# Optimization experiments

Hardware: AMD Instinct MI355X
Metric: run time of the kernel (lower is better)

Reference implementation:

```python
import jax, jax.numpy as jnp
import numpy as np

BN_EPS = 1e-5


def setup_inputs() -> dict:
    key = jax.random.key(0)
    k1, k2, k3 = jax.random.split(key, 3)
    N, C_in, T, V = 32, 64, 288, 25
    C_out = 64
    fv = jax.random.normal(k1, (N, C_in, T, V), dtype=jnp.float32)
    adj = jax.random.uniform(k2, (V, V), dtype=jnp.float32)
    # Conv2d(2*C_in, C_out, 1x1) weight flattened to [C_out, 2*C_in]; kaiming-ish scale
    W = jax.random.normal(k3, (C_out, 2 * C_in), dtype=jnp.float32) * (2.0 / (2 * C_in)) ** 0.5
    b = jnp.zeros((C_out,), dtype=jnp.float32)
    gamma = jnp.ones((C_out,), dtype=jnp.float32)   # bn_init scale=1
    beta = jnp.zeros((C_out,), dtype=jnp.float32)
    return {"fv": fv, "adj": adj, "W": W, "b": b, "gamma": gamma, "beta": beta}


def reference(fv, adj, W, b, gamma, beta):
    # fv: [N, C, T, V]; neighbor aggregation over joints via learnable adjacency
    fv_agg = jnp.einsum('nctv,vy->ncty', fv, adj)
    cat = jnp.concatenate([fv, fv_agg], axis=1)            # [N, 2C, T, V]
    # 1x1 conv == channel matmul
    out = jnp.einsum('ncty,oc->noty', cat, W) + b[None, :, None, None]
    # BatchNorm2d in training mode: batch stats over (N, T, V) per channel
    mean = out.mean(axis=(0, 2, 3), keepdims=True)
    var = out.var(axis=(0, 2, 3), keepdims=True)
    out = (out - mean) * jax.lax.rsqrt(var + BN_EPS)
    out = out * gamma[None, :, None, None] + beta[None, :, None, None]
    return jax.nn.relu(out)
```

## Files before the change

kernel.cpp:

```cpp
#include <hip/hip_runtime.h>

#define N_DIM 32
#define C_IN 64
#define C_OUT 64
#define T_DIM 288
#define V_DIM 25
#define TV 7200
#define NROWS 9216
#define NTV 230400
#define TOTAL 14745600
#define BN_EPS 1e-5f
#define NTILES 1800

#define WS_WINT 0
#define WS_SUM 8192
#define WS_SQ  8256

__global__ __launch_bounds__(256) void prep_kernel(const float* __restrict__ W,
                                                   float* __restrict__ ws) {
  const int i = blockIdx.x * 256 + threadIdx.x;
  if (blockIdx.x == 0 && threadIdx.x < 128) ws[WS_SUM + threadIdx.x] = 0.0f;
  const int s = i & 1;
  const int oo = (i >> 1) & 31;
  const int c = (i >> 6) & 63;
  const int h = i >> 12;
  const int o = h * 32 + oo;
  ws[WS_WINT + i] = W[o * 128 + s * 64 + c];
}

__device__ __forceinline__ float reduce32_lane(float* v, int lane) {
#pragma unroll
  for (int s = 0; s < 5; ++s) {
    const int m = 1 << s;
    const bool up = (lane & m) != 0;
    const int pairs = 32 >> (s + 1);
#pragma unroll
    for (int q = 0; q < pairs; ++q) {
      const float keep = up ? v[2 * q + 1] : v[2 * q];
      const float send = up ? v[2 * q] : v[2 * q + 1];
      const float recv = __shfl_xor(send, m, 64);
      v[q] = keep + recv;
    }
  }
  return v[0];
}

__global__ __launch_bounds__(256, 4) void main_kernel(
    const float* __restrict__ fv, const float* __restrict__ adj,
    const float* __restrict__ wint, float* __restrict__ stats,
    float* __restrict__ out) {
  __shared__ __align__(16) float buf[2][7][36];
  __shared__ float lsum[C_OUT];
  __shared__ float lsq[C_OUT];

  const int tid = threadIdx.x;
  if (tid < 64) { lsum[tid] = 0.0f; lsq[tid] = 0.0f; }

  const int half = __builtin_amdgcn_readfirstlane(tid) >> 7;
  const int lane = tid & 63;
  const float* __restrict__ wbase = wint + half * 4096;

  const int j0 = blockIdx.x << 7;
  const int col = j0 + (tid & 127);
  const int row = col / V_DIM;
  const int y = col - row * V_DIM;
  const int rbase = j0 / V_DIM;
  const int rowoff = row - rbase;

  float adjcol[V_DIM];
#pragma unroll
  for (int v = 0; v < V_DIM; ++v) adjcol[v] = adj[v * V_DIM + y];

  bool stager = false;
  int base_e = 0, srr = 0, sv = 0;
  if (tid < 175) {
    srr = tid / V_DIM;
    sv = tid - srr * V_DIM;
    const int Rg = rbase + srr;
    if (Rg < NROWS) {
      stager = true;
      const int n = Rg / T_DIM;
      const int t = Rg - n * T_DIM;
      base_e = n * (C_IN * TV) + t * V_DIM + sv;
    }
  }

  float acc[32];
#pragma unroll
  for (int oo = 0; oo < 32; ++oo) acc[oo] = 0.0f;

  float r0 = stager ? fv[base_e] : 0.0f;
  float r1 = stager ? fv[base_e + TV] : 0.0f;

#pragma unroll 1
  for (int c = 0; c < C_IN; ++c) {
    if (tid < 175) buf[c & 1][srr][sv] = r0;
    r0 = r1;
    if (stager && c + 2 < C_IN) r1 = fv[base_e + (c + 2) * TV];
    __syncthreads();

    const float* __restrict__ br = &buf[c & 1][rowoff][0];
    const float x = br[y];
    const float4* __restrict__ b4 = reinterpret_cast<const float4*>(br);
    float xa0 = 0.f, xa1 = 0.f, xa2 = 0.f, xa3 = 0.f;
#pragma unroll
    for (int q = 0; q < 6; ++q) {
      const float4 f = b4[q];
      xa0 = fmaf(f.x, adjcol[4 * q + 0], xa0);
      xa1 = fmaf(f.y, adjcol[4 * q + 1], xa1);
      xa2 = fmaf(f.z, adjcol[4 * q + 2], xa2);
      xa3 = fmaf(f.w, adjcol[4 * q + 3], xa3);
    }
    xa0 = fmaf(br[24], adjcol[24], xa0);
    const float xa = (xa0 + xa1) + (xa2 + xa3);

    const float* __restrict__ w = wbase + c * 64;
#pragma unroll
    for (int oo = 0; oo < 32; ++oo)
      acc[oo] = fmaf(x, w[oo * 2], fmaf(xa, w[oo * 2 + 1], acc[oo]));
  }

  {
    const int n = row / T_DIM;
    const int t = row - n * T_DIM;
    float* op = out + ((size_t)n * C_OUT + half * 32) * TV + t * V_DIM + y;
#pragma unroll
    for (int oo = 0; oo < 32; ++oo) op[oo * TV] = acc[oo];
  }

  float sq[32];
#pragma unroll
  for (int i = 0; i < 32; ++i) sq[i] = acc[i] * acc[i];
  float s = reduce32_lane(acc, lane);
  s += __shfl_xor(s, 32, 64);
  float q = reduce32_lane(sq, lane);
  q += __shfl_xor(q, 32, 64);

  if (lane < 32) {
    atomicAdd(&lsum[half * 32 + lane], s);
    atomicAdd(&lsq[half * 32 + lane], q);
  }
  __syncthreads();
  if (tid < 64) {
    atomicAdd(&stats[tid], lsum[tid]);
    atomicAdd(&stats[64 + tid], lsq[tid]);
  }
}

__global__ __launch_bounds__(256) void bn_kernel(const float* __restrict__ stats,
                                                 const float* __restrict__ gamma,
                                                 const float* __restrict__ beta,
                                                 float* __restrict__ out) {
  __shared__ float s_scale[C_OUT];
  __shared__ float s_shift[C_OUT];
  const int tid = threadIdx.x;
  if (tid < C_OUT) {
    const float inv = 1.0f / (float)NTV;
    const float mean = stats[tid] * inv;
    const float var = fmaf(stats[64 + tid], inv, -mean * mean);
    const float sc = gamma[tid] * rsqrtf(var + BN_EPS);
    s_scale[tid] = sc;
    s_shift[tid] = fmaf(-mean, sc, beta[tid]);
  }
  __syncthreads();

  float4* o4 = reinterpret_cast<float4*>(out);
  const int total4 = TOTAL / 4;
  const int stride = gridDim.x * blockDim.x;
  for (int i = blockIdx.x * blockDim.x + tid; i < total4; i += stride) {
    float4 v = o4[i];
    const int o = (i / 1800) & 63;
    const float sc = s_scale[o];
    const float sh = s_shift[o];
    v.x = fmaxf(fmaf(v.x, sc, sh), 0.0f);
    v.y = fmaxf(fmaf(v.y, sc, sh), 0.0f);
    v.z = fmaxf(fmaf(v.z, sc, sh), 0.0f);
    v.w = fmaxf(fmaf(v.w, sc, sh), 0.0f);
    o4[i] = v;
  }
}

extern "C" void kernel_launch(void* const* d_in, const int* in_sizes, int n_in,
                              void* d_out, int out_size, void* d_ws, size_t ws_size,
                              hipStream_t stream) {
  const float* fv = (const float*)d_in[0];
  const float* adj = (const float*)d_in[1];
  const float* W = (const float*)d_in[2];
  const float* gamma = (const float*)d_in[4];
  const float* beta = (const float*)d_in[5];
  float* out = (float*)d_out;
  float* ws = (float*)d_ws;

  hipLaunchKernelGGL(prep_kernel, dim3(32), dim3(256), 0, stream, W, ws);
  hipLaunchKernelGGL(main_kernel, dim3(NTILES), dim3(256), 0, stream,
                     fv, adj, ws + WS_WINT, ws + WS_SUM, out);
  hipLaunchKernelGGL(bn_kernel, dim3(2048), dim3(256), 0, stream,
                     ws + WS_SUM, gamma, beta, out);
}
```

Measured before the change: 298.3 us.

## Stage full per-tile fv slab in LDS once and simplify BN pass indexing

The main kernel no longer double-buffers one channel at a time with a barrier per channel. It now loads all 64 channels of the tile's fv slab into shared memory up front, with a single sync before the compute loop. This removes 64 barriers and exposes more memory-level parallelism, but uses about 50KB of LDS per block and lowers the launch-bounds occupancy hint from 4 to 3. The BN kernel now assigns one (n,channel) plane per block and computes scale and shift per block, dropping the shared-memory table and the per-element divide.

Measured after the change: 286.4 us. -4.0%, faster.

```diff
diff --git a/kernel.cpp b/kernel.cpp
--- a/kernel.cpp
+++ b/kernel.cpp
@@ -11,6 +11,9 @@
 #define TOTAL 14745600
 #define BN_EPS 1e-5f
 #define NTILES 1800
+
+#define ROW_W 28
+#define SLAB_W 196
 
 #define WS_WINT 0
 #define WS_SUM 8192
@@ -45,11 +48,11 @@
   return v[0];
 }
 
-__global__ __launch_bounds__(256, 4) void main_kernel(
+__global__ __launch_bounds__(256, 3) void fused_kernel(
     const float* __restrict__ fv, const float* __restrict__ adj,
     const float* __restrict__ wint, float* __restrict__ stats,
     float* __restrict__ out) {
-  __shared__ __align__(16) float buf[2][7][36];
+  __shared__ __align__(16) float lfv[C_IN * SLAB_W];
   __shared__ float lsum[C_OUT];
   __shared__ float lsq[C_OUT];
 
@@ -61,45 +64,40 @@
   const float* __restrict__ wbase = wint + half * 4096;
 
   const int j0 = blockIdx.x << 7;
+  const int rbase = j0 / V_DIM;
   const int col = j0 + (tid & 127);
   const int row = col / V_DIM;
   const int y = col - row * V_DIM;
-  const int rbase = j0 / V_DIM;
   const int rowoff = row - rbase;
 
   float adjcol[V_DIM];
 #pragma unroll
   for (int v = 0; v < V_DIM; ++v) adjcol[v] = adj[v * V_DIM + y];
 
-  bool stager = false;
-  int base_e = 0, srr = 0, sv = 0;
-  if (tid < 175) {
-    srr = tid / V_DIM;
-    sv = tid - srr * V_DIM;
-    const int Rg = rbase + srr;
+#pragma unroll 1
+  for (int i = tid; i < C_IN * 175; i += 256) {
+    const int c = i / 175;
+    const int rem = i - c * 175;
+    const int rr = rem / V_DIM;
+    const int v = rem - rr * V_DIM;
+    const int Rg = rbase + rr;
+    float val = 0.0f;
     if (Rg < NROWS) {
-      stager = true;
       const int n = Rg / T_DIM;
       const int t = Rg - n * T_DIM;
-      base_e = n * (C_IN * TV) + t * V_DIM + sv;
+      val = fv[n * (C_IN * TV) + c * TV + t * V_DIM + v];
     }
+    lfv[c * SLAB_W + rr * ROW_W + v] = val;
   }
+  __syncthreads();
 
   float acc[32];
 #pragma unroll
   for (int oo = 0; oo < 32; ++oo) acc[oo] = 0.0f;
 
-  float r0 = stager ? fv[base_e] : 0.0f;
-  float r1 = stager ? fv[base_e + TV] : 0.0f;
-
 #pragma unroll 1
   for (int c = 0; c < C_IN; ++c) {
-    if (tid < 175) buf[c & 1][srr][sv] = r0;
-    r0 = r1;
-    if (stager && c + 2 < C_IN) r1 = fv[base_e + (c + 2) * TV];
-    __syncthreads();
-
-    const float* __restrict__ br = &buf[c & 1][rowoff][0];
+    const float* __restrict__ br = &lfv[c * SLAB_W + rowoff * ROW_W];
     const float x = br[y];
     const float4* __restrict__ b4 = reinterpret_cast<const float4*>(br);
     float xa0 = 0.f, xa1 = 0.f, xa2 = 0.f, xa3 = 0.f;
@@ -151,32 +149,22 @@
                                                  const float* __restrict__ gamma,
                                                  const float* __restrict__ beta,
                                                  float* __restrict__ out) {
-  __shared__ float s_scale[C_OUT];
-  __shared__ float s_shift[C_OUT];
-  const int tid = threadIdx.x;
-  if (tid < C_OUT) {
-    const float inv = 1.0f / (float)NTV;
-    const float mean = stats[tid] * inv;
-    const float var = fmaf(stats[64 + tid], inv, -mean * mean);
-    const float sc = gamma[tid] * rsqrtf(var + BN_EPS);
-    s_scale[tid] = sc;
-    s_shift[tid] = fmaf(-mean, sc, beta[tid]);
-  }
-  __syncthreads();
+  const int o = blockIdx.x & 63;
+  const float inv = 1.0f / (float)NTV;
+  const float mean = stats[o] * inv;
+  const float var = fmaf(stats[64 + o], inv, -mean * mean);
+  const float sc = gamma[o] * rsqrtf(var + BN_EPS);
+  const float sh = fmaf(-mean, sc, beta[o]);
 
-  float4* o4 = reinterpret_cast<float4*>(out);
-  const int total4 = TOTAL / 4;
-  const int stride = gridDim.x * blockDim.x;
-  for (int i = blockIdx.x * blockDim.x + tid; i < total4; i += stride) {
-    float4 v = o4[i];
-    const int o = (i / 1800) & 63;
-    const float sc = s_scale[o];
-    const float sh = s_shift[o];
+  float4* base = reinterpret_cast<float4*>(out) + (size_t)blockIdx.x * 1800;
+#pragma unroll 1
+  for (int i = threadIdx.x; i < 1800; i += 256) {
+    float4 v = base[i];
     v.x = fmaxf(fmaf(v.x, sc, sh), 0.0f);
     v.y = fmaxf(fmaf(v.y, sc, sh), 0.0f);
     v.z = fmaxf(fmaf(v.z, sc, sh), 0.0f);
     v.w = fmaxf(fmaf(v.w, sc, sh), 0.0f);
-    o4[i] = v;
+    base[i] = v;
   }
 }
 
@@ -192,8 +180,8 @@
   float* ws = (float*)d_ws;
 
   hipLaunchKernelGGL(prep_kernel, dim3(32), dim3(256), 0, stream, W, ws);
-  hipLaunchKernelGGL(main_kernel, dim3(NTILES), dim3(256), 0, stream,
+  hipLaunchKernelGGL(fused_kernel, dim3(NTILES), dim3(256), 0, stream,
                      fv, adj, ws + WS_WINT, ws + WS_SUM, out);
-  hipLaunchKernelGGL(bn_kernel, dim3(2048), dim3(256), 0, stream,
+  hipLaunchKernelGGL(bn_kernel, dim3(N_DIM * C_OUT), dim3(256), 0, stream,
                      ws + WS_SUM, gamma, beta, out);
 }
```
